# Kernel tuning notes

Hardware: AMD Instinct MI355X
Metric: run time of the kernel (lower is better)

## Reference

```python
import jax, jax.numpy as jnp
import numpy as np

T, B, E, H = 1024, 4, 1024, 16
D = E // H  # head_dim = 64


def rel_shift(x):
    # Transformer-XL relative shift trick (RelativeShift.forward, batch_first=True).
    # x: [BH, Q, P] -> pad one zero column, reshape [BH, P+1, Q], drop first row, reshape back.
    BH, Q, P = x.shape
    zp = jnp.zeros((BH, Q, 1), x.dtype)
    xp = jnp.concatenate([zp, x], axis=2).reshape(BH, P + 1, Q)
    return xp[:, 1:, :].reshape(BH, Q, P)


def setup_inputs() -> dict:
    key = jax.random.key(0)
    ks = jax.random.split(key, 8)
    std = float(np.sqrt(2.0 / (E + E)))
    causal = jnp.triu(jnp.ones((T, T), dtype=bool), k=1)  # True = masked (future positions)
    return {
        "x": jax.random.normal(ks[0], (T, B, E), dtype=jnp.float32),
        "pos": jax.random.normal(ks[1], (T, 1, E), dtype=jnp.float32),
        "in_proj_weight": jax.random.normal(ks[2], (3 * E, E), dtype=jnp.float32) * std,
        "in_proj_bias": jnp.zeros((3 * E,), dtype=jnp.float32),
        "out_proj_weight": jax.random.normal(ks[3], (E, E), dtype=jnp.float32) * std,
        "out_proj_bias": jnp.zeros((E,), dtype=jnp.float32),
        "pos_proj_weight": jax.random.normal(ks[4], (E, E), dtype=jnp.float32) * std,
        "pos_proj_bias": jnp.zeros((E,), dtype=jnp.float32),
        "r_w_bias": jax.random.normal(ks[5], (H, D), dtype=jnp.float32) * 0.02,
        "r_r_bias": jax.random.normal(ks[6], (H, D), dtype=jnp.float32) * 0.02,
        "attn_mask": causal,
    }


def reference(x, pos, in_proj_weight, in_proj_bias, out_proj_weight, out_proj_bias,
              pos_proj_weight, pos_proj_bias, r_w_bias, r_r_bias, attn_mask):
    Tq, Bb, Ee = x.shape
    scale = 1.0 / np.sqrt(D).astype(np.float32)
    # fused QKV projection; layout [T, B, heads, 3, head_dim] matches
    # view(len_q, bsz*heads, 3, head_dim) in the original.
    qkv = (x @ in_proj_weight.T + in_proj_bias).reshape(Tq, Bb, H, 3, D)
    q = qkv[..., 0, :]  # [T,B,H,D]
    k = qkv[..., 1, :]
    v = qkv[..., 2, :]
    # position projection (shared across batch since pos is [T,1,E])
    r_head_k = (pos[:, 0, :] @ pos_proj_weight.T + pos_proj_bias).reshape(Tq, H, D)  # [P,H,D]
    rw_q = q + r_w_bias  # content bias
    rr_q = q + r_r_bias  # position bias
    ac = jnp.einsum('qbhd,kbhd->bhqk', rw_q, k) * scale            # [B,H,Q,K]
    bd = jnp.einsum('qbhd,phd->bhqp', rr_q, r_head_k) * scale      # [B,H,Q,P]
    bd = rel_shift(bd.reshape(Bb * H, Tq, Tq)).reshape(Bb, H, Tq, Tq)[..., :Tq]
    score = ac + bd
    score = jnp.where(attn_mask[None, None, :, :], -jnp.inf, score)
    attn = jax.nn.softmax(score, axis=-1)                          # [B,H,Q,K]
    ctx = jnp.einsum('bhqk,kbhd->qbhd', attn, v).reshape(Tq, Bb, Ee)
    out = ctx @ out_proj_weight.T + out_proj_bias                  # [T,B,E]
    return out, attn
```

## Files before the change

### kernel.cpp

```cpp
#include <hip/hip_runtime.h>
#include <math.h>

#define TQ 1024
#define BBATCH 4
#define EDIM 1024
#define HHEADS 16
#define DHEAD 64

typedef __bf16 bf16x8 __attribute__((ext_vector_type(8)));
typedef __bf16 bf16x4 __attribute__((ext_vector_type(4)));
typedef float  f32x4  __attribute__((ext_vector_type(4)));

#define LDK 40

template<int MODE>
__global__ __launch_bounds__(256) void gemm_mfma_abt(
    const float* __restrict__ A, const float* __restrict__ B,
    const float* __restrict__ bias, float* __restrict__ C,
    int M, int N, int K)
{
    __shared__ __bf16 As[128 * LDK];
    __shared__ __bf16 Bs[128 * LDK];
    const int tid  = threadIdx.x;
    const int lane = tid & 63;
    const int wid  = tid >> 6;
    const int wr   = wid >> 1, wc = wid & 1;
    const int m0 = blockIdx.y * 128, n0 = blockIdx.x * 128;

    f32x4 acc[4][4] = {};

    const int sm0 = tid >> 2;
    const int sm1 = sm0 + 64;
    const int sk  = (tid & 3) << 3;

    const int fr = lane & 15;
    const int kg = (lane >> 4) << 3;

    for (int k0 = 0; k0 < K; k0 += 32) {
        float4 ra0a = *(const float4*)&A[(size_t)(m0 + sm0) * K + k0 + sk];
        float4 ra0b = *(const float4*)&A[(size_t)(m0 + sm0) * K + k0 + sk + 4];
        float4 ra1a = *(const float4*)&A[(size_t)(m0 + sm1) * K + k0 + sk];
        float4 ra1b = *(const float4*)&A[(size_t)(m0 + sm1) * K + k0 + sk + 4];
        float4 rb0a = *(const float4*)&B[(size_t)(n0 + sm0) * K + k0 + sk];
        float4 rb0b = *(const float4*)&B[(size_t)(n0 + sm0) * K + k0 + sk + 4];
        float4 rb1a = *(const float4*)&B[(size_t)(n0 + sm1) * K + k0 + sk];
        float4 rb1b = *(const float4*)&B[(size_t)(n0 + sm1) * K + k0 + sk + 4];

        __syncthreads();

        bf16x8 w;
        w[0]=(__bf16)ra0a.x; w[1]=(__bf16)ra0a.y; w[2]=(__bf16)ra0a.z; w[3]=(__bf16)ra0a.w;
        w[4]=(__bf16)ra0b.x; w[5]=(__bf16)ra0b.y; w[6]=(__bf16)ra0b.z; w[7]=(__bf16)ra0b.w;
        *(bf16x8*)&As[sm0 * LDK + sk] = w;
        w[0]=(__bf16)ra1a.x; w[1]=(__bf16)ra1a.y; w[2]=(__bf16)ra1a.z; w[3]=(__bf16)ra1a.w;
        w[4]=(__bf16)ra1b.x; w[5]=(__bf16)ra1b.y; w[6]=(__bf16)ra1b.z; w[7]=(__bf16)ra1b.w;
        *(bf16x8*)&As[sm1 * LDK + sk] = w;
        w[0]=(__bf16)rb0a.x; w[1]=(__bf16)rb0a.y; w[2]=(__bf16)rb0a.z; w[3]=(__bf16)rb0a.w;
        w[4]=(__bf16)rb0b.x; w[5]=(__bf16)rb0b.y; w[6]=(__bf16)rb0b.z; w[7]=(__bf16)rb0b.w;
        *(bf16x8*)&Bs[sm0 * LDK + sk] = w;
        w[0]=(__bf16)rb1a.x; w[1]=(__bf16)rb1a.y; w[2]=(__bf16)rb1a.z; w[3]=(__bf16)rb1a.w;
        w[4]=(__bf16)rb1b.x; w[5]=(__bf16)rb1b.y; w[6]=(__bf16)rb1b.z; w[7]=(__bf16)rb1b.w;
        *(bf16x8*)&Bs[sm1 * LDK + sk] = w;

        __syncthreads();

        bf16x8 af[4], bfr[4];
        #pragma unroll
        for (int i = 0; i < 4; ++i) {
            af[i]  = *(const bf16x8*)&As[(wr * 64 + i * 16 + fr) * LDK + kg];
            bfr[i] = *(const bf16x8*)&Bs[(wc * 64 + i * 16 + fr) * LDK + kg];
        }
        #pragma unroll
        for (int mi = 0; mi < 4; ++mi)
        #pragma unroll
        for (int ni = 0; ni < 4; ++ni)
            acc[mi][ni] = __builtin_amdgcn_mfma_f32_16x16x32_bf16(
                af[mi], bfr[ni], acc[mi][ni], 0, 0, 0);
    }

    const int fq = lane >> 4;
    #pragma unroll
    for (int mi = 0; mi < 4; ++mi)
    #pragma unroll
    for (int ni = 0; ni < 4; ++ni) {
        int row = m0 + wr * 64 + mi * 16 + fq * 4;
        int col = n0 + wc * 64 + ni * 16 + fr;
        float bv = bias[col];
        #pragma unroll
        for (int j = 0; j < 4; ++j) {
            float v = acc[mi][ni][j] + bv;
            if (MODE == 0) {
                C[(size_t)(row + j) * N + col] = v;
            } else {
                C[(((size_t)(col >> 6) << 10) + (row + j)) * 64 + (col & 63)] = v;
            }
        }
    }
}

__global__ __launch_bounds__(256) void bias_dots_kernel(
    const float* __restrict__ qkv, const float* __restrict__ Rm,
    const float* __restrict__ rwb, const float* __restrict__ rrb,
    float* __restrict__ cK, float* __restrict__ cR)
{
    int id = blockIdx.x * 256 + threadIdx.x;
    if (id < 65536) {
        int bh = id >> 10, k = id & 1023;
        int b = bh >> 4, h = bh & 15;
        const float* p = &qkv[((size_t)k * 4 + b) * 3072 + h * 192 + 64];
        const float* w = &rwb[h << 6];
        float s = 0.f;
        #pragma unroll
        for (int d = 0; d < 64; d += 4) {
            float4 v = *(const float4*)&p[d];
            s += v.x * w[d] + v.y * w[d + 1] + v.z * w[d + 2] + v.w * w[d + 3];
        }
        cK[id] = s;
    } else if (id < 81920) {
        int id2 = id - 65536;
        int h = id2 >> 10, j = id2 & 1023;
        const float* p = &Rm[(((size_t)h << 10) + j) * 64];
        const float* w = &rrb[h << 6];
        float s = 0.f;
        #pragma unroll
        for (int d = 0; d < 64; d += 4) {
            float4 v = *(const float4*)&p[d];
            s += v.x * w[d] + v.y * w[d + 1] + v.z * w[d + 2] + v.w * w[d + 3];
        }
        cR[id2] = s;
    }
}

#define SLD 72

__global__ __launch_bounds__(256) void score_tile_kernel(
    const float* __restrict__ qkv, const float* __restrict__ Rm,
    const float* __restrict__ cK, const float* __restrict__ cR,
    float* __restrict__ attn, float2* __restrict__ part)
{
    int t = blockIdx.x;
    int qt = (int)((sqrtf(8.f * t + 1.f) - 1.f) * 0.5f);
    while ((qt + 1) * (qt + 2) / 2 <= t) ++qt;
    while (qt * (qt + 1) / 2 > t) --qt;
    int kt = t - qt * (qt + 1) / 2;

    const int bh = blockIdx.y;
    const int b = bh >> 4, h = bh & 15;
    const int q0 = qt << 6, k0 = kt << 6;
    const int tid = threadIdx.x, lane = tid & 63, wid = tid >> 6;
    const int fr = lane & 15, fq = lane >> 4, kg = fq << 3;
    const int w16 = wid << 4;
    const int base_j = k0 - q0 + 960;

    __shared__ __align__(16) char smem[36864];
    __bf16* Qs = (__bf16*)smem;
    __bf16* Ks = (__bf16*)(smem + 9216);
    __bf16* R0 = (__bf16*)(smem + 18432);
    __bf16* R1 = (__bf16*)(smem + 27648);
    float (*BDs)[68] = (float(*)[68])smem;

    float4 qreg[4], kreg[4], r0reg[4], r1reg[4];
    #pragma unroll
    for (int s = 0; s < 4; ++s) {
        int idx = (s << 8) + tid;
        int r = idx >> 4, dc = (idx & 15) << 2;
        qreg[s] = *(const float4*)&qkv[((size_t)(q0 + r) * 4 + b) * 3072 + h * 192 + dc];
        kreg[s] = *(const float4*)&qkv[((size_t)(k0 + r) * 4 + b) * 3072 + h * 192 + 64 + dc];
        int j0 = base_j + r;       if (j0 > 1023) j0 = 1023;
        int j1 = base_j + 64 + r;  if (j1 > 1023) j1 = 1023;
        r0reg[s] = *(const float4*)&Rm[(((size_t)h << 10) + j0) * 64 + dc];
        r1reg[s] = *(const float4*)&Rm[(((size_t)h << 10) + j1) * 64 + dc];
    }
    #pragma unroll
    for (int s = 0; s < 4; ++s) {
        int idx = (s << 8) + tid;
        int r = idx >> 4, dc = (idx & 15) << 2;
        bf16x4 w;
        w[0]=(__bf16)qreg[s].x; w[1]=(__bf16)qreg[s].y; w[2]=(__bf16)qreg[s].z; w[3]=(__bf16)qreg[s].w;
        *(bf16x4*)&Qs[r * SLD + dc] = w;
        w[0]=(__bf16)kreg[s].x; w[1]=(__bf16)kreg[s].y; w[2]=(__bf16)kreg[s].z; w[3]=(__bf16)kreg[s].w;
        *(bf16x4*)&Ks[r * SLD + dc] = w;
        w[0]=(__bf16)r0reg[s].x; w[1]=(__bf16)r0reg[s].y; w[2]=(__bf16)r0reg[s].z; w[3]=(__bf16)r0reg[s].w;
        *(bf16x4*)&R0[r * SLD + dc] = w;
        w[0]=(__bf16)r1reg[s].x; w[1]=(__bf16)r1reg[s].y; w[2]=(__bf16)r1reg[s].z; w[3]=(__bf16)r1reg[s].w;
        *(bf16x4*)&R1[r * SLD + dc] = w;
    }
    __syncthreads();

    bf16x8 af0 = *(const bf16x8*)&Qs[(w16 + fr) * SLD + kg];
    bf16x8 af1 = *(const bf16x8*)&Qs[(w16 + fr) * SLD + 32 + kg];

    f32x4 aac[4], abd[4];
    const f32x4 z4 = {0.f, 0.f, 0.f, 0.f};

    #pragma unroll
    for (int ni = 0; ni < 4; ++ni) {
        bf16x8 b0 = *(const bf16x8*)&Ks[(ni * 16 + fr) * SLD + kg];
        bf16x8 b1 = *(const bf16x8*)&Ks[(ni * 16 + fr) * SLD + 32 + kg];
        aac[ni] = __builtin_amdgcn_mfma_f32_16x16x32_bf16(af0, b0, z4, 0, 0, 0);
        aac[ni] = __builtin_amdgcn_mfma_f32_16x16x32_bf16(af1, b1, aac[ni], 0, 0, 0);
    }
    #pragma unroll
    for (int ni = 0; ni < 4; ++ni) {
        bf16x8 b0 = *(const bf16x8*)&R0[(ni * 16 + fr) * SLD + kg];
        bf16x8 b1 = *(const bf16x8*)&R0[(ni * 16 + fr) * SLD + 32 + kg];
        abd[ni] = __builtin_amdgcn_mfma_f32_16x16x32_bf16(af0, b0, z4, 0, 0, 0);
        abd[ni] = __builtin_amdgcn_mfma_f32_16x16x32_bf16(af1, b1, abd[ni], 0, 0, 0);
    }

    __syncthreads();

    #pragma unroll
    for (int ni = 0; ni < 4; ++ni)
    #pragma unroll
    for (int j = 0; j < 4; ++j)
        BDs[w16 + fq * 4 + j][ni * 16 + fr] = abd[ni][j];
    asm volatile("s_waitcnt lgkmcnt(0)" ::: "memory");
    #pragma unroll
    for (int ni = 0; ni < 4; ++ni)
    #pragma unroll
    for (int j = 0; j < 4; ++j) {
        int lrow = w16 + fq * 4 + j;
        int widx = (ni * 16 + fr) - lrow + 63;
        if (widx < 64) aac[ni][j] += BDs[lrow][widx];
    }
    asm volatile("s_waitcnt lgkmcnt(0)" ::: "memory");

    #pragma unroll
    for (int ni = 0; ni < 4; ++ni) {
        bf16x8 b0 = *(const bf16x8*)&R1[(ni * 16 + fr) * SLD + kg];
        bf16x8 b1 = *(const bf16x8*)&R1[(ni * 16 + fr) * SLD + 32 + kg];
        abd[ni] = __builtin_amdgcn_mfma_f32_16x16x32_bf16(af0, b0, z4, 0, 0, 0);
        abd[ni] = __builtin_amdgcn_mfma_f32_16x16x32_bf16(af1, b1, abd[ni], 0, 0, 0);
    }
    #pragma unroll
    for (int ni = 0; ni < 4; ++ni)
    #pragma unroll
    for (int j = 0; j < 4; ++j)
        BDs[w16 + fq * 4 + j][ni * 16 + fr] = abd[ni][j];
    asm volatile("s_waitcnt lgkmcnt(0)" ::: "memory");
    #pragma unroll
    for (int ni = 0; ni < 4; ++ni)
    #pragma unroll
    for (int j = 0; j < 4; ++j) {
        int lrow = w16 + fq * 4 + j;
        int widx = (ni * 16 + fr) - lrow + 63;
        if (widx >= 64) aac[ni][j] += BDs[lrow][widx - 64];
    }

    float sc[4][4];
    #pragma unroll
    for (int ni = 0; ni < 4; ++ni) {
        int lcol = ni * 16 + fr;
        int k = k0 + lcol;
        float ckv = cK[(bh << 10) + k];
        #pragma unroll
        for (int j = 0; j < 4; ++j) {
            int lrow = w16 + fq * 4 + j;
            int q = q0 + lrow;
            int widx = lcol - lrow + 63;
            int jidx = base_j + widx; if (jidx > 1023) jidx = 1023;
            float crv = cR[(h << 10) + jidx];
            float v = 0.125f * (aac[ni][j] + ckv + crv);
            if (kt == qt && lcol > lrow) v = -1e30f;
            sc[ni][j] = v;
            attn[((((size_t)bh << 10) + q) << 10) + k] = v;
        }
    }
    #pragma unroll
    for (int j = 0; j < 4; ++j) {
        float tmax = fmaxf(fmaxf(sc[0][j], sc[1][j]), fmaxf(sc[2][j], sc[3][j]));
        tmax = fmaxf(tmax, __shfl_xor(tmax, 1));
        tmax = fmaxf(tmax, __shfl_xor(tmax, 2));
        tmax = fmaxf(tmax, __shfl_xor(tmax, 4));
        tmax = fmaxf(tmax, __shfl_xor(tmax, 8));
        float ps = __expf(sc[0][j] - tmax) + __expf(sc[1][j] - tmax)
                 + __expf(sc[2][j] - tmax) + __expf(sc[3][j] - tmax);
        ps += __shfl_xor(ps, 1); ps += __shfl_xor(ps, 2);
        ps += __shfl_xor(ps, 4); ps += __shfl_xor(ps, 8);
        if (fr == 0)
            part[(((size_t)(bh << 10) + q0 + w16 + fq * 4 + j) << 4) + kt]
                = make_float2(tmax, ps);
    }
}

__global__ __launch_bounds__(256) void stats_reduce_kernel(
    const float2* __restrict__ part, float2* __restrict__ stats)
{
    const int row = blockIdx.x * 256 + threadIdx.x;
    const int q = row & 1023;
    const int nt = (q >> 6) + 1;
    float2 pr[16];
    float m = -1e30f;
    for (int kt = 0; kt < nt; ++kt) {
        pr[kt] = part[((size_t)row << 4) + kt];
        m = fmaxf(m, pr[kt].x);
    }
    float s = 0.f;
    for (int kt = 0; kt < nt; ++kt)
        s += pr[kt].y * __expf(pr[kt].x - m);
    stats[row] = make_float2(m, 1.0f / s);
}

#define FLD 66

__global__ __launch_bounds__(256) void ctx_norm_kernel(
    const float* __restrict__ qkv, const float2* __restrict__ stats,
    float* __restrict__ attn, float* __restrict__ ctx)
{
    const int qt = 15 - blockIdx.x;
    const int bh = blockIdx.y;
    const int b = bh >> 4, h = bh & 15;
    const int q0 = qt << 6;
    const int tid = threadIdx.x, lane = tid & 63, wid = tid >> 6;
    const int fr = lane & 15, fq = lane >> 4, kg = fq << 3;
    const int w16 = wid << 4;

    __shared__ __bf16 Pl[64 * FLD];
    __shared__ __bf16 Vt[64 * FLD];

    float mrow[4], inv[4];
    #pragma unroll
    for (int j = 0; j < 4; ++j) {
        float2 st = stats[(bh << 10) + q0 + w16 + fq * 4 + j];
        mrow[j] = st.x; inv[j] = st.y;
    }

    f32x4 apv[4] = {};
    for (int kt = 0; kt <= qt; ++kt) {
        const int k0 = kt << 6;
        float4 vreg[4];
        #pragma unroll
        for (int s = 0; s < 4; ++s) {
            int idx = (s << 8) + tid, r = idx >> 4, dc = (idx & 15) << 2;
            vreg[s] = *(const float4*)&qkv[((size_t)(k0 + r) * 4 + b) * 3072 + h * 192 + 128 + dc];
        }
        float praw[4][4];
        #pragma unroll
        for (int ni = 0; ni < 4; ++ni)
        #pragma unroll
        for (int j = 0; j < 4; ++j)
            praw[ni][j] = attn[((size_t)bh << 20) +
                               ((size_t)(q0 + w16 + fq * 4 + j) << 10) + k0 + ni * 16 + fr];
        __syncthreads();
        #pragma unroll
        for (int s = 0; s < 4; ++s) {
            int idx = (s << 8) + tid, r = idx >> 4, dc = (idx & 15) << 2;
            Vt[(dc + 0) * FLD + r] = (__bf16)vreg[s].x;
            Vt[(dc + 1) * FLD + r] = (__bf16)vreg[s].y;
            Vt[(dc + 2) * FLD + r] = (__bf16)vreg[s].z;
            Vt[(dc + 3) * FLD + r] = (__bf16)vreg[s].w;
        }
        #pragma unroll
        for (int ni = 0; ni < 4; ++ni)
        #pragma unroll
        for (int j = 0; j < 4; ++j) {
            float p = __expf(praw[ni][j] - mrow[j]) * inv[j];
            attn[((size_t)bh << 20) +
                 ((size_t)(q0 + w16 + fq * 4 + j) << 10) + k0 + ni * 16 + fr] = p;
            Pl[(w16 + fq * 4 + j) * FLD + ni * 16 + fr] = (__bf16)p;
        }
        __syncthreads();
        bf16x8 pa0 = *(const bf16x8*)&Pl[(w16 + fr) * FLD + kg];
        bf16x8 pa1 = *(const bf16x8*)&Pl[(w16 + fr) * FLD + 32 + kg];
        #pragma unroll
        for (int ni = 0; ni < 4; ++ni) {
            bf16x8 bv0 = *(const bf16x8*)&Vt[(ni * 16 + fr) * FLD + kg];
            bf16x8 bv1 = *(const bf16x8*)&Vt[(ni * 16 + fr) * FLD + 32 + kg];
            apv[ni] = __builtin_amdgcn_mfma_f32_16x16x32_bf16(pa0, bv0, apv[ni], 0, 0, 0);
            apv[ni] = __builtin_amdgcn_mfma_f32_16x16x32_bf16(pa1, bv1, apv[ni], 0, 0, 0);
        }
    }

    for (int kt = qt + 1; kt < 16; ++kt) {
        const int k0 = kt << 6;
        #pragma unroll
        for (int s = 0; s < 4; ++s) {
            int idx = (s << 8) + tid, r = idx >> 4, c4 = (idx & 15) << 2;
            float4 z = {0.f, 0.f, 0.f, 0.f};
            *(float4*)&attn[((size_t)bh << 20) + ((size_t)(q0 + r) << 10) + k0 + c4] = z;
        }
    }
    #pragma unroll
    for (int ni = 0; ni < 4; ++ni)
    #pragma unroll
    for (int j = 0; j < 4; ++j)
        ctx[((size_t)(q0 + w16 + fq * 4 + j) * 4 + b) * 1024 + (h << 6) + ni * 16 + fr]
            = apv[ni][j];
}

extern "C" void kernel_launch(void* const* d_in, const int* in_sizes, int n_in,
                              void* d_out, int out_size, void* d_ws, size_t ws_size,
                              hipStream_t stream)
{
    (void)in_sizes; (void)n_in; (void)out_size; (void)ws_size;
    const float* x     = (const float*)d_in[0];
    const float* pos   = (const float*)d_in[1];
    const float* w_in  = (const float*)d_in[2];
    const float* b_in  = (const float*)d_in[3];
    const float* w_out = (const float*)d_in[4];
    const float* b_out = (const float*)d_in[5];
    const float* w_pos = (const float*)d_in[6];
    const float* b_pos = (const float*)d_in[7];
    const float* rwb   = (const float*)d_in[8];
    const float* rrb   = (const float*)d_in[9];

    float* out  = (float*)d_out;
    float* attn = out + (size_t)TQ * BBATCH * EDIM;

    float* ws  = (float*)d_ws;
    float* qkv = ws;
    float* R   = qkv + (size_t)4096 * 3072;
    float* ctx = R + (size_t)HHEADS * TQ * DHEAD;
    float*  cK    = out;
    float*  cR    = out + 65536;
    float2* stats = (float2*)(out + 81920);
    float2* part  = (float2*)(out + 262144);

    dim3 blk(256, 1, 1);

    gemm_mfma_abt<0><<<dim3(3072 / 128, 4096 / 128), blk, 0, stream>>>(
        x, w_in, b_in, qkv, 4096, 3072, 1024);
    gemm_mfma_abt<1><<<dim3(1024 / 128, 1024 / 128), blk, 0, stream>>>(
        pos, w_pos, b_pos, R, 1024, 1024, 1024);
    bias_dots_kernel<<<dim3(320), blk, 0, stream>>>(qkv, R, rwb, rrb, cK, cR);
    score_tile_kernel<<<dim3(136, 64), blk, 0, stream>>>(qkv, R, cK, cR, attn, part);
    stats_reduce_kernel<<<dim3(256), blk, 0, stream>>>(part, stats);
    ctx_norm_kernel<<<dim3(16, 64), blk, 0, stream>>>(qkv, stats, attn, ctx);
    gemm_mfma_abt<0><<<dim3(1024 / 128, 4096 / 128), blk, 0, stream>>>(
        ctx, w_out, b_out, out, 4096, 1024, 1024);
}
```

Baseline: 379.7 us.

## Split ctx normalization across two K halves with atomic accumulation

The causal P·V kernel now launches two blocks per query tile, each covering half of the key tiles, and merges partial context results with atomicAdd into a ctx buffer that the stats kernel zeroes first. This targets load imbalance and low parallelism from triangular work. The attn read/normalize/write also moves to a row-major float4 access pattern so the global loads and stores coalesce. The cost is extra atomic traffic on ctx and a ctx zeroing pass.

```diff
diff --git a/kernel.cpp b/kernel.cpp
--- a/kernel.cpp
+++ b/kernel.cpp
@@ -285,7 +285,8 @@
 }
 
 __global__ __launch_bounds__(256) void stats_reduce_kernel(
-    const float2* __restrict__ part, float2* __restrict__ stats)
+    const float2* __restrict__ part, float2* __restrict__ stats,
+    float* __restrict__ ctx)
 {
     const int row = blockIdx.x * 256 + threadIdx.x;
     const int q = row & 1023;
@@ -300,65 +301,73 @@
     for (int kt = 0; kt < nt; ++kt)
         s += pr[kt].y * __expf(pr[kt].x - m);
     stats[row] = make_float2(m, 1.0f / s);
+
+    const float4 z = {0.f, 0.f, 0.f, 0.f};
+    #pragma unroll
+    for (int i = 0; i < 16; ++i)
+        *(float4*)&ctx[((size_t)i * 65536 + row) * 4] = z;
 }
 
 #define FLD 66
 
-__global__ __launch_bounds__(256) void ctx_norm_kernel(
+__global__ __launch_bounds__(256) void ctx_split_kernel(
     const float* __restrict__ qkv, const float2* __restrict__ stats,
     float* __restrict__ attn, float* __restrict__ ctx)
 {
-    const int qt = 15 - blockIdx.x;
+    const int pid = blockIdx.x;
+    const int qt = 15 - (pid >> 1);
+    const int half = pid & 1;
+    const int n = qt + 1;
+    const int nh0 = (n + 1) >> 1;
+    const int kts = half ? nh0 : 0;
+    const int kte = half ? n : nh0;
+
     const int bh = blockIdx.y;
     const int b = bh >> 4, h = bh & 15;
     const int q0 = qt << 6;
     const int tid = threadIdx.x, lane = tid & 63, wid = tid >> 6;
     const int fr = lane & 15, fq = lane >> 4, kg = fq << 3;
     const int w16 = wid << 4;
+    const int c4 = (tid & 15) << 2;
+    const int rb = tid >> 4;
 
     __shared__ __bf16 Pl[64 * FLD];
     __shared__ __bf16 Vt[64 * FLD];
 
     float mrow[4], inv[4];
     #pragma unroll
-    for (int j = 0; j < 4; ++j) {
-        float2 st = stats[(bh << 10) + q0 + w16 + fq * 4 + j];
-        mrow[j] = st.x; inv[j] = st.y;
+    for (int s = 0; s < 4; ++s) {
+        float2 st = stats[(bh << 10) + q0 + rb + (s << 4)];
+        mrow[s] = st.x; inv[s] = st.y;
     }
 
     f32x4 apv[4] = {};
-    for (int kt = 0; kt <= qt; ++kt) {
+    for (int kt = kts; kt < kte; ++kt) {
         const int k0 = kt << 6;
-        float4 vreg[4];
+        float4 vreg[4], praw[4];
         #pragma unroll
         for (int s = 0; s < 4; ++s) {
-            int idx = (s << 8) + tid, r = idx >> 4, dc = (idx & 15) << 2;
-            vreg[s] = *(const float4*)&qkv[((size_t)(k0 + r) * 4 + b) * 3072 + h * 192 + 128 + dc];
-        }
-        float praw[4][4];
-        #pragma unroll
-        for (int ni = 0; ni < 4; ++ni)
-        #pragma unroll
-        for (int j = 0; j < 4; ++j)
-            praw[ni][j] = attn[((size_t)bh << 20) +
-                               ((size_t)(q0 + w16 + fq * 4 + j) << 10) + k0 + ni * 16 + fr];
+            int r = rb + (s << 4);
+            vreg[s] = *(const float4*)&qkv[((size_t)(k0 + r) * 4 + b) * 3072 + h * 192 + 128 + c4];
+            praw[s] = *(const float4*)&attn[((size_t)bh << 20) + ((size_t)(q0 + r) << 10) + k0 + c4];
+        }
         __syncthreads();
         #pragma unroll
         for (int s = 0; s < 4; ++s) {
-            int idx = (s << 8) + tid, r = idx >> 4, dc = (idx & 15) << 2;
-            Vt[(dc + 0) * FLD + r] = (__bf16)vreg[s].x;
-            Vt[(dc + 1) * FLD + r] = (__bf16)vreg[s].y;
-            Vt[(dc + 2) * FLD + r] = (__bf16)vreg[s].z;
-            Vt[(dc + 3) * FLD + r] = (__bf16)vreg[s].w;
-        }
-        #pragma unroll
-        for (int ni = 0; ni < 4; ++ni)
-        #pragma unroll
-        for (int j = 0; j < 4; ++j) {
-            float p = __expf(praw[ni][j] - mrow[j]) * inv[j];
-            attn[((size_t)bh << 20) +
-                 ((size_t)(q0 + w16 + fq * 4 + j) << 10) + k0 + ni * 16 + fr] = p;
-            Pl[(w16 + fq * 4 + j) * FLD + ni * 16 + fr] = (__bf16)p;
+            int r = rb + (s << 4);
+            Vt[(c4 + 0) * FLD + r] = (__bf16)vreg[s].x;
+            Vt[(c4 + 1) * FLD + r] = (__bf16)vreg[s].y;
+            Vt[(c4 + 2) * FLD + r] = (__bf16)vreg[s].z;
+            Vt[(c4 + 3) * FLD + r] = (__bf16)vreg[s].w;
+            float4 p;
+            p.x = __expf(praw[s].x - mrow[s]) * inv[s];
+            p.y = __expf(praw[s].y - mrow[s]) * inv[s];
+            p.z = __expf(praw[s].z - mrow[s]) * inv[s];
+            p.w = __expf(praw[s].w - mrow[s]) * inv[s];
+            *(float4*)&attn[((size_t)bh << 20) + ((size_t)(q0 + r) << 10) + k0 + c4] = p;
+            bf16x4 pw;
+            pw[0]=(__bf16)p.x; pw[1]=(__bf16)p.y; pw[2]=(__bf16)p.z; pw[3]=(__bf16)p.w;
+            *(bf16x4*)&Pl[r * FLD + c4] = pw;
         }
         __syncthreads();
         bf16x8 pa0 = *(const bf16x8*)&Pl[(w16 + fr) * FLD + kg];
@@ -372,21 +381,26 @@
         }
     }
 
-    for (int kt = qt + 1; kt < 16; ++kt) {
-        const int k0 = kt << 6;
-        #pragma unroll
-        for (int s = 0; s < 4; ++s) {
-            int idx = (s << 8) + tid, r = idx >> 4, c4 = (idx & 15) << 2;
-            float4 z = {0.f, 0.f, 0.f, 0.f};
-            *(float4*)&attn[((size_t)bh << 20) + ((size_t)(q0 + r) << 10) + k0 + c4] = z;
-        }
-    }
-    #pragma unroll
-    for (int ni = 0; ni < 4; ++ni)
-    #pragma unroll
-    for (int j = 0; j < 4; ++j)
-        ctx[((size_t)(q0 + w16 + fq * 4 + j) * 4 + b) * 1024 + (h << 6) + ni * 16 + fr]
-            = apv[ni][j];
+    if (half) {
+        for (int kt = n; kt < 16; ++kt) {
+            const int k0 = kt << 6;
+            #pragma unroll
+            for (int s = 0; s < 4; ++s) {
+                int r = rb + (s << 4);
+                float4 z = {0.f, 0.f, 0.f, 0.f};
+                *(float4*)&attn[((size_t)bh << 20) + ((size_t)(q0 + r) << 10) + k0 + c4] = z;
+            }
+        }
+    }
+
+    if (kte > kts) {
+        #pragma unroll
+        for (int ni = 0; ni < 4; ++ni)
+        #pragma unroll
+        for (int j = 0; j < 4; ++j)
+            atomicAdd(&ctx[((size_t)(q0 + w16 + fq * 4 + j) * 4 + b) * 1024
+                           + (h << 6) + ni * 16 + fr], apv[ni][j]);
+    }
 }
 
 extern "C" void kernel_launch(void* const* d_in, const int* in_sizes, int n_in,
@@ -425,8 +439,8 @@
         pos, w_pos, b_pos, R, 1024, 1024, 1024);
     bias_dots_kernel<<<dim3(320), blk, 0, stream>>>(qkv, R, rwb, rrb, cK, cR);
     score_tile_kernel<<<dim3(136, 64), blk, 0, stream>>>(qkv, R, cK, cR, attn, part);
-    stats_reduce_kernel<<<dim3(256), blk, 0, stream>>>(part, stats);
-    ctx_norm_kernel<<<dim3(16, 64), blk, 0, stream>>>(qkv, stats, attn, ctx);
+    stats_reduce_kernel<<<dim3(256), blk, 0, stream>>>(part, stats, ctx);
+    ctx_split_kernel<<<dim3(32, 64), blk, 0, stream>>>(qkv, stats, attn, ctx);
     gemm_mfma_abt<0><<<dim3(1024 / 128, 4096 / 128), blk, 0, stream>>>(
         ctx, w_out, b_out, out, 4096, 1024, 1024);
 }
```

Measured after the change: 376.1 us. About the same (-0.9%).
